# Optimization experiments

Hardware: AMD Instinct MI355X
Metric: run time of the kernel (lower is better)

The kernel has to match this reference:

```python
import jax, jax.numpy as jnp
import numpy as np

N_NODES = 500_000
N_EDGES = 16_000_000


def setup_inputs() -> dict:
    key = jax.random.key(0)
    ks = jax.random.split(key, 16)
    x = jax.random.normal(ks[0], (N_NODES, 4), dtype=jnp.float32)
    edge_index = jax.random.randint(ks[1], (2, N_EDGES), 0, N_NODES, dtype=jnp.int64)

    def lin(k, out_dim, in_dim):
        # kaiming-uniform-ish init like torch Linear
        bound = 1.0 / np.sqrt(in_dim)
        return jax.random.uniform(k, (out_dim, in_dim), jnp.float32, -bound, bound)

    def bias(k, out_dim, in_dim):
        bound = 1.0 / np.sqrt(in_dim)
        return jax.random.uniform(k, (out_dim,), jnp.float32, -bound, bound)

    return {
        "x": x,
        "edge_index": edge_index,
        # SAGEConv1: 4 -> 10  (lin_l acts on aggregated neighbors, has bias; lin_r on self, no bias)
        "w1l": lin(ks[2], 10, 4), "b1": bias(ks[3], 10, 4), "w1r": lin(ks[4], 10, 4),
        # SAGEConv2: 10 -> 20
        "w2l": lin(ks[5], 20, 10), "b2": bias(ks[6], 20, 10), "w2r": lin(ks[7], 20, 10),
        # SAGEConv3: 20 -> 20
        "w3l": lin(ks[8], 20, 20), "b3": bias(ks[9], 20, 20), "w3r": lin(ks[10], 20, 20),
        # classifier: 20 -> 8
        "wc": lin(ks[11], 8, 20), "bc": bias(ks[12], 8, 20),
    }


def _sage_conv(h, src, dst, deg_inv, wl, bl, wr):
    # mean-aggregate neighbor features: messages flow src -> dst
    msg = h[src]                                   # [E, F] gather
    agg = jax.ops.segment_sum(msg, dst, num_segments=N_NODES)  # [N, F]
    agg = agg * deg_inv                            # mean over in-neighbors
    return agg @ wl.T + bl + h @ wr.T              # lin_l(aggr) + lin_r(self)


def reference(x, edge_index, w1l, b1, w1r, w2l, b2, w2r, w3l, b3, w3r, wc, bc):
    src, dst = edge_index[0], edge_index[1]
    deg = jax.ops.segment_sum(jnp.ones((src.shape[0],), x.dtype), dst,
                              num_segments=N_NODES)
    deg_inv = (1.0 / jnp.maximum(deg, 1.0))[:, None]  # [N, 1]

    h = jax.nn.relu(_sage_conv(x, src, dst, deg_inv, w1l, b1, w1r))
    h = jax.nn.relu(_sage_conv(h, src, dst, deg_inv, w2l, b2, w2r))
    h = jax.nn.relu(_sage_conv(h, src, dst, deg_inv, w3l, b3, w3r))
    return h @ wc.T + bc
```

## Files before the change

### kernel.cpp

```cpp
#include <hip/hip_runtime.h>
#include <hip/hip_fp16.h>

#define N_NODES 500000
#define N_EDGES 16000000
#define NB 1954
#define NPB_LOG 9
#define NPB 512
#define NBUCK 977
#define NBUCK_PAD 1024
#define CH 16384
#define NSB 977

#define SLICE_SHIFT 15
#define NSLICE 16
#define NKEY (NPB * NSLICE)

#define GRID_BLK 1024
#define HALF_T (GRID_BLK * 256)

#define BAR_SUBC 16
#define BAR_SUBQ (GRID_BLK / BAR_SUBC)
#define BAR_REC_INTS 1024
#define BAR_MASTER 512
#define BAR_FLAG 544
#define ENTRY_BUDGET 1500
#define PHASE_BUDGET 400

__device__ __forceinline__ float2 up2(int p) {
    __half2 h = *reinterpret_cast<__half2*>(&p);
    return __half22float2(h);
}
__device__ __forceinline__ int pk2(float a, float b) {
    __half2 h = __floats2half2_rn(a, b);
    return *reinterpret_cast<int*>(&h);
}

__device__ __forceinline__ void barrier_arrive(int* rec, int bid) {
    int r = __hip_atomic_fetch_add(&rec[(bid & (BAR_SUBC - 1)) * 32], 1,
                                   __ATOMIC_RELAXED, __HIP_MEMORY_SCOPE_AGENT);
    if (r == BAR_SUBQ - 1) {
        int mr = __hip_atomic_fetch_add(&rec[BAR_MASTER], 1,
                                        __ATOMIC_RELAXED, __HIP_MEMORY_SCOPE_AGENT);
        if (mr == BAR_SUBC - 1)
            __hip_atomic_store(&rec[BAR_FLAG], 1,
                               __ATOMIC_RELAXED, __HIP_MEMORY_SCOPE_AGENT);
    }
}
__device__ __forceinline__ bool barrier_wait(int* rec, int budget) {
    int spins = 0;
    while (__hip_atomic_load(&rec[BAR_FLAG],
                             __ATOMIC_RELAXED, __HIP_MEMORY_SCOPE_AGENT) == 0) {
        if (++spins > budget) return false;
        __builtin_amdgcn_s_sleep(8);
    }
    return true;
}


__global__ void bucket_hist(const int* __restrict__ dst, int* __restrict__ ghist) {
    __shared__ int lhist[NBUCK_PAD];
    for (int t = threadIdx.x; t < NBUCK_PAD; t += 256) lhist[t] = 0;
    __syncthreads();
    int stride = gridDim.x * 256;
    for (int i = blockIdx.x * 256 + threadIdx.x; i < N_EDGES; i += stride) {
        atomicAdd(&lhist[dst[i] >> NPB_LOG], 1);
    }
    __syncthreads();
    for (int t = threadIdx.x; t < NBUCK_PAD; t += 256) {
        int c = lhist[t];
        if (c) atomicAdd(&ghist[t], c);
    }
}

__global__ void bucket_scan(int* __restrict__ gcur, int* __restrict__ bbase) {
    __shared__ int s[256];
    int t = threadIdx.x;
    int v[4], sum = 0, loc[4];
#pragma unroll
    for (int j = 0; j < 4; ++j) {
        v[j] = gcur[t * 4 + j];
        loc[j] = sum;
        sum += v[j];
    }
    s[t] = sum;
    __syncthreads();
    for (int o = 1; o < 256; o <<= 1) {
        int x = (t >= o) ? s[t - o] : 0;
        __syncthreads();
        s[t] += x;
        __syncthreads();
    }
    int excl = s[t] - sum;
#pragma unroll
    for (int j = 0; j < 4; ++j) {
        int e = excl + loc[j];
        bbase[t * 4 + j] = e;
        gcur[t * 4 + j] = e;
    }
    if (t == 255) bbase[NBUCK_PAD] = s[255];
}

__global__ __launch_bounds__(256) void bucket_scatter(
        const int* __restrict__ src, const int* __restrict__ dst,
        int* __restrict__ gcur, int* __restrict__ P) {
    __shared__ int lP[CH];
    __shared__ int lhist[NBUCK_PAD];
    __shared__ int lexcl[NBUCK_PAD];
    __shared__ int gbase[NBUCK_PAD];
    __shared__ int sscan[256];
    int t = threadIdx.x;
    for (int j = t; j < NBUCK_PAD; j += 256) lhist[j] = 0;
    __syncthreads();

    int e0 = blockIdx.x * CH;
    int e1 = min(e0 + CH, N_EDGES);
    for (int i = e0 + t; i < e1; i += 256) {
        atomicAdd(&lhist[dst[i] >> NPB_LOG], 1);
    }
    __syncthreads();

    int base4 = t * 4;
    int c[4], sum = 0;
#pragma unroll
    for (int j = 0; j < 4; ++j) { c[j] = lhist[base4 + j]; sum += c[j]; }
#pragma unroll
    for (int j = 0; j < 4; ++j) {
        gbase[base4 + j] = c[j] ? atomicAdd(&gcur[base4 + j], c[j]) : 0;
    }
    sscan[t] = sum;
    __syncthreads();
    for (int o = 1; o < 256; o <<= 1) {
        int x = (t >= o) ? sscan[t - o] : 0;
        __syncthreads();
        sscan[t] += x;
        __syncthreads();
    }
    int run = sscan[t] - sum;
#pragma unroll
    for (int j = 0; j < 4; ++j) {
        lexcl[base4 + j] = run;
        lhist[base4 + j] = run;
        run += c[j];
    }
    __syncthreads();

    for (int i = e0 + t; i < e1; i += 256) {
        int d = dst[i];
        int s = src[i];
        int b = d >> NPB_LOG;
        int pos = atomicAdd(&lhist[b], 1);
        lP[pos] = ((d & (NPB - 1)) << 19) | s;
    }
    __syncthreads();

    int wave = t >> 6, lane = t & 63;
    for (int b = wave; b < NBUCK_PAD; b += 4) {
        int lb = lexcl[b];
        int cnt = lhist[b] - lb;
        int gb = gbase[b];
        for (int j = lane; j < cnt; j += 64) {
            P[gb + j] = lP[lb + j];
        }
    }
}

__global__ void fine_sort(const int* __restrict__ P, const int* __restrict__ bbase,
                          int* __restrict__ off, int* __restrict__ S) {
    __shared__ int hist[NKEY];
    __shared__ int sscan[256];
    int t = threadIdx.x;
    int b = blockIdx.x;
    int bb = bbase[b];
    int be = bbase[b + 1];
    int node0 = b << NPB_LOG;

    for (int j = t; j < NKEY; j += 256) hist[j] = 0;
    __syncthreads();
    for (int j = bb + t; j < be; j += 256) {
        int p = P[j];
        int n = p >> 19;
        int s = p & 0x7FFFF;
        atomicAdd(&hist[(n << 4) | (s >> SLICE_SHIFT)], 1);
    }
    __syncthreads();

    int base = t * 32;
    int sum = 0;
#pragma unroll
    for (int j = 0; j < 32; ++j) sum += hist[base + j];
    sscan[t] = sum;
    __syncthreads();
    for (int o = 1; o < 256; o <<= 1) {
        int x = (t >= o) ? sscan[t - o] : 0;
        __syncthreads();
        sscan[t] += x;
        __syncthreads();
    }
    int run = sscan[t] - sum;
#pragma unroll
    for (int j = 0; j < 32; ++j) {
        int c = hist[base + j];
        hist[base + j] = run;
        run += c;
    }
    __syncthreads();

#pragma unroll
    for (int j = 0; j < 2; ++j) {
        int idx = t + j * 256;
        int ng = node0 + idx;
        if (ng < N_NODES) off[ng] = bb + hist[idx << 4];
    }
    if (b == NBUCK - 1 && t == 0) off[N_NODES] = N_EDGES;
    __syncthreads();

    for (int j = bb + t; j < be; j += 256) {
        int p = P[j];
        int n = p >> 19;
        int s = p & 0x7FFFF;
        int pos = atomicAdd(&hist[(n << 4) | (s >> SLICE_SHIFT)], 1);
        S[bb + pos] = s;
    }
}

__global__ __launch_bounds__(256) void count_slices(const int* __restrict__ off,
        const int* __restrict__ S, int4* __restrict__ cnt8) {
    int i = blockIdx.x * 256 + threadIdx.x;
    if (i >= N_NODES) return;
    int b = off[i], e = off[i + 1];
    int w0 = 0, w1 = 0, w2 = 0, w3 = 0;
    for (int k = b; k < e; ++k) {
        int sl = S[k] >> SLICE_SHIFT;
        int inc = 1 << ((sl & 3) * 8);
        if (sl < 8) { if (sl < 4) w0 += inc; else w1 += inc; }
        else        { if (sl < 12) w2 += inc; else w3 += inc; }
    }
    cnt8[i] = make_int4(w0, w1, w2, w3);
}


__global__ void convert_x(const float* __restrict__ x, int2* __restrict__ xh) {
    int i = blockIdx.x * 256 + threadIdx.x;
    if (i >= N_NODES) return;
    float4 v = ((const float4*)x)[i];
    int2 r;
    r.x = pk2(v.x, v.y);
    r.y = pk2(v.z, v.w);
    xh[i] = r;
}


__global__ __launch_bounds__(256, 4) void fused_l1(
        const int* __restrict__ off, const int* __restrict__ ssrc,
        const int2* __restrict__ xh, const float* __restrict__ x,
        const float* __restrict__ wl, const float* __restrict__ bl,
        const float* __restrict__ wr, int* __restrict__ h1) {
    __shared__ float s_wl[40];
    __shared__ float s_wr[40];
    __shared__ float s_b[10];
    if (threadIdx.x < 40) {
        s_wl[threadIdx.x] = wl[threadIdx.x];
        s_wr[threadIdx.x] = wr[threadIdx.x];
    }
    if (threadIdx.x >= 64 && threadIdx.x < 74) s_b[threadIdx.x - 64] = bl[threadIdx.x - 64];
    __syncthreads();

    int i = blockIdx.x * 256 + threadIdx.x;
    if (i >= N_NODES) return;

    int b = off[i], e = off[i + 1];
    constexpr int UN = 8;

    float acc[4] = {0.f, 0.f, 0.f, 0.f};

    int k = b;
    for (; k + UN - 1 < e; k += UN) {
        int sidx[UN];
#pragma unroll
        for (int u = 0; u < UN; ++u) sidx[u] = ssrc[k + u];
        int2 v[UN];
#pragma unroll
        for (int u = 0; u < UN; ++u) v[u] = xh[sidx[u]];
#pragma unroll
        for (int u = 0; u < UN; ++u) {
            float2 f0 = up2(v[u].x), f1 = up2(v[u].y);
            acc[0] += f0.x; acc[1] += f0.y; acc[2] += f1.x; acc[3] += f1.y;
        }
    }
    for (; k < e; ++k) {
        int2 v = xh[ssrc[k]];
        float2 f0 = up2(v.x), f1 = up2(v.y);
        acc[0] += f0.x; acc[1] += f0.y; acc[2] += f1.x; acc[3] += f1.y;
    }

    float inv = 1.f / fmaxf((float)(e - b), 1.f);
#pragma unroll
    for (int q = 0; q < 4; ++q) acc[q] *= inv;

    float4 xs = ((const float4*)x)[i];
    float xv[4] = {xs.x, xs.y, xs.z, xs.w};

    float r[10];
#pragma unroll
    for (int j = 0; j < 10; ++j) {
        float t = s_b[j];
#pragma unroll
        for (int kk = 0; kk < 4; ++kk) {
            t += s_wl[j * 4 + kk] * acc[kk] + s_wr[j * 4 + kk] * xv[kk];
        }
        r[j] = fmaxf(t, 0.f);
    }
    int4 o0;
    o0.x = pk2(r[0], r[1]); o0.y = pk2(r[2], r[3]);
    o0.z = pk2(r[4], r[5]); o0.w = pk2(r[6], r[7]);
    *(int4*)(h1 + (long)i * 8) = o0;
    h1[(long)i * 8 + 4] = pk2(r[8], r[9]);
}


__device__ __forceinline__ void l2_scan_m(int& k, int m,
        const int* __restrict__ ssrc, const int* __restrict__ h1, float* acc) {
    for (; m >= 4; m -= 4, k += 4) {
        int sidx[4];
#pragma unroll
        for (int u = 0; u < 4; ++u) sidx[u] = ssrc[k + u];
        int4 v4[4];
        int v1[4];
#pragma unroll
        for (int u = 0; u < 4; ++u) {
            const int* row = h1 + (long)sidx[u] * 8;
            v4[u] = *(const int4*)row;
            v1[u] = row[4];
        }
#pragma unroll
        for (int u = 0; u < 4; ++u) {
            float2 f0 = up2(v4[u].x), f1 = up2(v4[u].y), f2 = up2(v4[u].z),
                   f3 = up2(v4[u].w), f4 = up2(v1[u]);
            acc[0] += f0.x; acc[1] += f0.y; acc[2] += f1.x; acc[3] += f1.y;
            acc[4] += f2.x; acc[5] += f2.y; acc[6] += f3.x; acc[7] += f3.y;
            acc[8] += f4.x; acc[9] += f4.y;
        }
    }
    for (; m > 0; --m, ++k) {
        const int* row = h1 + (long)ssrc[k] * 8;
        int4 v4 = *(const int4*)row;
        int v1 = row[4];
        float2 f0 = up2(v4.x), f1 = up2(v4.y), f2 = up2(v4.z), f3 = up2(v4.w), f4 = up2(v1);
        acc[0] += f0.x; acc[1] += f0.y; acc[2] += f1.x; acc[3] += f1.y;
        acc[4] += f2.x; acc[5] += f2.y; acc[6] += f3.x; acc[7] += f3.y;
        acc[8] += f4.x; acc[9] += f4.y;
    }
}

__device__ __forceinline__ void l3_scan_m(int& k, int m,
        const int* __restrict__ ssrc, const int* __restrict__ h2, float* acc) {
    for (; m >= 4; m -= 4, k += 4) {
        int sidx[4];
#pragma unroll
        for (int u = 0; u < 4; ++u) sidx[u] = ssrc[k + u];
        int4 va[4], vb[4];
        int2 vc[4];
#pragma unroll
        for (int u = 0; u < 4; ++u) {
            const int* row = h2 + (long)sidx[u] * 16;
            va[u] = *(const int4*)row;
            vb[u] = *(const int4*)(row + 4);
            vc[u] = *(const int2*)(row + 8);
        }
#pragma unroll
        for (int u = 0; u < 4; ++u) {
            float2 f;
            f = up2(va[u].x); acc[0] += f.x; acc[1] += f.y;
            f = up2(va[u].y); acc[2] += f.x; acc[3] += f.y;
            f = up2(va[u].z); acc[4] += f.x; acc[5] += f.y;
            f = up2(va[u].w); acc[6] += f.x; acc[7] += f.y;
            f = up2(vb[u].x); acc[8] += f.x; acc[9] += f.y;
            f = up2(vb[u].y); acc[10] += f.x; acc[11] += f.y;
            f = up2(vb[u].z); acc[12] += f.x; acc[13] += f.y;
            f = up2(vb[u].w); acc[14] += f.x; acc[15] += f.y;
            f = up2(vc[u].x); acc[16] += f.x; acc[17] += f.y;
            f = up2(vc[u].y); acc[18] += f.x; acc[19] += f.y;
        }
    }
    for (; m > 0; --m, ++k) {
        const int* row = h2 + (long)ssrc[k] * 16;
        int4 va = *(const int4*)row;
        int4 vb = *(const int4*)(row + 4);
        int2 vc = *(const int2*)(row + 8);
        float2 f;
        f = up2(va.x); acc[0] += f.x; acc[1] += f.y;
        f = up2(va.y); acc[2] += f.x; acc[3] += f.y;
        f = up2(va.z); acc[4] += f.x; acc[5] += f.y;
        f = up2(va.w); acc[6] += f.x; acc[7] += f.y;
        f = up2(vb.x); acc[8] += f.x; acc[9] += f.y;
        f = up2(vb.y); acc[10] += f.x; acc[11] += f.y;
        f = up2(vb.z); acc[12] += f.x; acc[13] += f.y;
        f = up2(vb.w); acc[14] += f.x; acc[15] += f.y;
        f = up2(vc.x); acc[16] += f.x; acc[17] += f.y;
        f = up2(vc.y); acc[18] += f.x; acc[19] += f.y;
    }
}

__device__ __forceinline__ void l2_tail(int n, float deg, float* acc,
        const int* __restrict__ h1, const float* s_wl, const float* s_wr,
        const float* s_b, int* __restrict__ h2) {
    if (n >= N_NODES) return;
    float inv = 1.f / fmaxf(deg, 1.f);
#pragma unroll
    for (int q = 0; q < 10; ++q) acc[q] *= inv;
    float xv[10];
    {
        const int* row = h1 + (long)n * 8;
        int4 v4 = *(const int4*)row;
        int v1 = row[4];
        float2 f0 = up2(v4.x), f1 = up2(v4.y), f2 = up2(v4.z), f3 = up2(v4.w), f4 = up2(v1);
        xv[0] = f0.x; xv[1] = f0.y; xv[2] = f1.x; xv[3] = f1.y;
        xv[4] = f2.x; xv[5] = f2.y; xv[6] = f3.x; xv[7] = f3.y;
        xv[8] = f4.x; xv[9] = f4.y;
    }
    float r[20];
#pragma unroll
    for (int j = 0; j < 20; ++j) {
        float t = s_b[j];
#pragma unroll
        for (int kk = 0; kk < 10; ++kk)
            t += s_wl[j * 10 + kk] * acc[kk] + s_wr[j * 10 + kk] * xv[kk];
        r[j] = fmaxf(t, 0.f);
    }
    int* o = h2 + (long)n * 16;
    int4 o0, o1;
    o0.x = pk2(r[0], r[1]);   o0.y = pk2(r[2], r[3]);
    o0.z = pk2(r[4], r[5]);   o0.w = pk2(r[6], r[7]);
    o1.x = pk2(r[8], r[9]);   o1.y = pk2(r[10], r[11]);
    o1.z = pk2(r[12], r[13]); o1.w = pk2(r[14], r[15]);
    *(int4*)o = o0;
    *(int4*)(o + 4) = o1;
    int2 o2;
    o2.x = pk2(r[16], r[17]); o2.y = pk2(r[18], r[19]);
    *(int2*)(o + 8) = o2;
}

__global__ __launch_bounds__(256, 4) void fused_l2p(
        const int* __restrict__ off, const int* __restrict__ ssrc,
        const int* __restrict__ h1,
        const float* __restrict__ wl, const float* __restrict__ bl,
        const float* __restrict__ wr, int* __restrict__ h2,
        const int4* __restrict__ cnt8, int* __restrict__ bar) {
    __shared__ float s_wl[200];
    __shared__ float s_wr[200];
    __shared__ float s_b[20];
    if (threadIdx.x < 200) {
        s_wl[threadIdx.x] = wl[threadIdx.x];
        s_wr[threadIdx.x] = wr[threadIdx.x];
    }
    if (threadIdx.x >= 224 && threadIdx.x < 244) s_b[threadIdx.x - 224] = bl[threadIdx.x - 224];
    __syncthreads();

    const int tg = blockIdx.x * 256 + threadIdx.x;
    const int n0 = tg, n1 = tg + HALF_T;
    int k0 = off[n0];
    float deg0 = (float)(off[n0 + 1] - k0);
    int4 c0 = cnt8[n0];
    int k1 = 0;
    float deg1 = 0.f;
    int4 c1 = make_int4(0, 0, 0, 0);
    if (n1 < N_NODES) {
        k1 = off[n1];
        deg1 = (float)(off[n1 + 1] - k1);
        c1 = cnt8[n1];
    }
    float acc0[10], acc1[10];
#pragma unroll
    for (int q = 0; q < 10; ++q) { acc0[q] = 0.f; acc1[q] = 0.f; }

    bool coop = true;
    if (threadIdx.x == 0) {
        barrier_arrive(bar, blockIdx.x);
        coop = barrier_wait(bar, ENTRY_BUDGET);
    }
    __syncthreads();

    constexpr int PH = 8;
    for (int s = 0; s < PH; ++s) {
        int cw0 = (s < 4) ? ((s < 2) ? c0.x : c0.y) : ((s < 6) ? c0.z : c0.w);
        int cw1 = (s < 4) ? ((s < 2) ? c1.x : c1.y) : ((s < 6) ? c1.z : c1.w);
        int sh = (s & 1) * 16;
        int m0 = ((cw0 >> sh) & 255) + ((cw0 >> (sh + 8)) & 255);
        int m1 = ((cw1 >> sh) & 255) + ((cw1 >> (sh + 8)) & 255);
        l2_scan_m(k0, m0, ssrc, h1, acc0);
        l2_scan_m(k1, m1, ssrc, h1, acc1);
        if (s < PH - 1) {
            if (threadIdx.x == 0) {
                int* rec = bar + (1 + s) * BAR_REC_INTS;
                barrier_arrive(rec, blockIdx.x);
                if (coop) coop = barrier_wait(rec, PHASE_BUDGET);
            }
            __syncthreads();
        }
    }
    l2_tail(n0, deg0, acc0, h1, s_wl, s_wr, s_b, h2);
    l2_tail(n1, deg1, acc1, h1, s_wl, s_wr, s_b, h2);
}

__device__ __forceinline__ void l3_tail(int n, float deg, float* acc,
        const int* __restrict__ h2, const float* s_wl, const float* s_wr,
        const float* s_b, const float* s_wc, const float* s_bc,
        float* __restrict__ out) {
    if (n >= N_NODES) return;
    float inv = 1.f / fmaxf(deg, 1.f);
#pragma unroll
    for (int q = 0; q < 20; ++q) acc[q] *= inv;
    float xv[20];
    {
        const int* row = h2 + (long)n * 16;
        int4 va = *(const int4*)row;
        int4 vb = *(const int4*)(row + 4);
        int2 vc = *(const int2*)(row + 8);
        float2 f;
        f = up2(va.x); xv[0] = f.x; xv[1] = f.y;
        f = up2(va.y); xv[2] = f.x; xv[3] = f.y;
        f = up2(va.z); xv[4] = f.x; xv[5] = f.y;
        f = up2(va.w); xv[6] = f.x; xv[7] = f.y;
        f = up2(vb.x); xv[8] = f.x; xv[9] = f.y;
        f = up2(vb.y); xv[10] = f.x; xv[11] = f.y;
        f = up2(vb.z); xv[12] = f.x; xv[13] = f.y;
        f = up2(vb.w); xv[14] = f.x; xv[15] = f.y;
        f = up2(vc.x); xv[16] = f.x; xv[17] = f.y;
        f = up2(vc.y); xv[18] = f.x; xv[19] = f.y;
    }
    float h3[20];
#pragma unroll
    for (int j = 0; j < 20; ++j) {
        float r = s_b[j];
#pragma unroll
        for (int kk = 0; kk < 20; ++kk)
            r += s_wl[j * 20 + kk] * acc[kk] + s_wr[j * 20 + kk] * xv[kk];
        h3[j] = fmaxf(r, 0.f);
    }
#pragma unroll
    for (int j = 0; j < 8; ++j) {
        float r = s_bc[j];
#pragma unroll
        for (int kk = 0; kk < 20; ++kk) r += s_wc[j * 20 + kk] * h3[kk];
        out[(long)n * 8 + j] = r;
    }
}

__global__ __launch_bounds__(256, 4) void fused_l3p(
        const int* __restrict__ off, const int* __restrict__ ssrc,
        const int* __restrict__ h2,
        const float* __restrict__ w3l, const float* __restrict__ b3,
        const float* __restrict__ w3r,
        const float* __restrict__ wc, const float* __restrict__ bc,
        float* __restrict__ out, const int4* __restrict__ cnt8,
        int* __restrict__ bar) {
    __shared__ float s_wl[400];
    __shared__ float s_wr[400];
    __shared__ float s_b[20];
    __shared__ float s_wc[160];
    __shared__ float s_bc[8];
    for (int t = threadIdx.x; t < 400; t += 256) {
        s_wl[t] = w3l[t];
        s_wr[t] = w3r[t];
    }
    if (threadIdx.x < 160) s_wc[threadIdx.x] = wc[threadIdx.x];
    if (threadIdx.x >= 192 && threadIdx.x < 212) s_b[threadIdx.x - 192] = b3[threadIdx.x - 192];
    if (threadIdx.x >= 224 && threadIdx.x < 232) s_bc[threadIdx.x - 224] = bc[threadIdx.x - 224];
    __syncthreads();

    const int tg = blockIdx.x * 256 + threadIdx.x;
    const int n0 = tg, n1 = tg + HALF_T;
    int k0 = off[n0];
    float deg0 = (float)(off[n0 + 1] - k0);
    int4 c0 = cnt8[n0];
    int k1 = 0;
    float deg1 = 0.f;
    int4 c1 = make_int4(0, 0, 0, 0);
    if (n1 < N_NODES) {
        k1 = off[n1];
        deg1 = (float)(off[n1 + 1] - k1);
        c1 = cnt8[n1];
    }
    float acc0[20], acc1[20];
#pragma unroll
    for (int q = 0; q < 20; ++q) { acc0[q] = 0.f; acc1[q] = 0.f; }

    bool coop = true;
    if (threadIdx.x == 0) {
        barrier_arrive(bar, blockIdx.x);
        coop = barrier_wait(bar, ENTRY_BUDGET);
    }
    __syncthreads();

    constexpr int PH = 16;
    for (int s = 0; s < PH; ++s) {
        int cw0 = (s < 8) ? ((s < 4) ? c0.x : c0.y) : ((s < 12) ? c0.z : c0.w);
        int cw1 = (s < 8) ? ((s < 4) ? c1.x : c1.y) : ((s < 12) ? c1.z : c1.w);
        int sh = (s & 3) * 8;
        int m0 = (cw0 >> sh) & 255;
        int m1 = (cw1 >> sh) & 255;
        l3_scan_m(k0, m0, ssrc, h2, acc0);
        l3_scan_m(k1, m1, ssrc, h2, acc1);
        if (s < PH - 1) {
            if (threadIdx.x == 0) {
                int* rec = bar + (1 + s) * BAR_REC_INTS;
                barrier_arrive(rec, blockIdx.x);
                if (coop) coop = barrier_wait(rec, PHASE_BUDGET);
            }
            __syncthreads();
        }
    }
    l3_tail(n0, deg0, acc0, h2, s_wl, s_wr, s_b, s_wc, s_bc, out);
    l3_tail(n1, deg1, acc1, h2, s_wl, s_wr, s_b, s_wc, s_bc, out);
}


__global__ void deg_kernel(const int* __restrict__ dst, int* __restrict__ deg) {
    int i = blockIdx.x * blockDim.x + threadIdx.x;
    if (i < N_EDGES) atomicAdd(&deg[dst[i]], 1);
}

template <int F>
__global__ void edge_agg(const int* __restrict__ src, const int* __restrict__ dst,
                         const float* __restrict__ h, float* __restrict__ agg) {
    int i = blockIdx.x * blockDim.x + threadIdx.x;
    if (i >= N_EDGES) return;
    int s = src[i];
    int d = dst[i];
    const float* hs = h + (long)s * F;
    float* ad = agg + (long)d * F;
#pragma unroll
    for (int f = 0; f < F; ++f) atomicAdd(&ad[f], hs[f]);
}

template <int FIN, int FOUT>
__global__ void node_apply(const float* __restrict__ agg, const float* __restrict__ hin,
                           const int* __restrict__ deg, const float* __restrict__ wl,
                           const float* __restrict__ bl, const float* __restrict__ wr,
                           float* __restrict__ hout) {
    __shared__ float s_wl[FOUT * FIN];
    __shared__ float s_wr[FOUT * FIN];
    __shared__ float s_b[FOUT];
    for (int t = threadIdx.x; t < FOUT * FIN; t += blockDim.x) {
        s_wl[t] = wl[t];
        s_wr[t] = wr[t];
    }
    for (int t = threadIdx.x; t < FOUT; t += blockDim.x) s_b[t] = bl[t];
    __syncthreads();
    int i = blockIdx.x * blockDim.x + threadIdx.x;
    if (i >= N_NODES) return;
    float inv = 1.0f / fmaxf((float)deg[i], 1.0f);
    float a[FIN], xv[FIN];
#pragma unroll
    for (int kk = 0; kk < FIN; ++kk) {
        a[kk] = agg[(long)i * FIN + kk] * inv;
        xv[kk] = hin[(long)i * FIN + kk];
    }
#pragma unroll
    for (int j = 0; j < FOUT; ++j) {
        float r = s_b[j];
#pragma unroll
        for (int kk = 0; kk < FIN; ++kk) r += s_wl[j * FIN + kk] * a[kk] + s_wr[j * FIN + kk] * xv[kk];
        hout[(long)i * FOUT + j] = fmaxf(r, 0.f);
    }
}

__global__ void node_final_old(const float* __restrict__ agg, const float* __restrict__ hin,
                               const int* __restrict__ deg, const float* __restrict__ w3l,
                               const float* __restrict__ b3, const float* __restrict__ w3r,
                               const float* __restrict__ wc, const float* __restrict__ bc,
                               float* __restrict__ out) {
    __shared__ float s_wl[400];
    __shared__ float s_wr[400];
    __shared__ float s_b[20];
    __shared__ float s_wc[160];
    __shared__ float s_bc[8];
    for (int t = threadIdx.x; t < 400; t += blockDim.x) {
        s_wl[t] = w3l[t];
        s_wr[t] = w3r[t];
    }
    for (int t = threadIdx.x; t < 160; t += blockDim.x) s_wc[t] = wc[t];
    for (int t = threadIdx.x; t < 20; t += blockDim.x) s_b[t] = b3[t];
    for (int t = threadIdx.x; t < 8; t += blockDim.x) s_bc[t] = bc[t];
    __syncthreads();
    int i = blockIdx.x * blockDim.x + threadIdx.x;
    if (i >= N_NODES) return;
    float inv = 1.0f / fmaxf((float)deg[i], 1.0f);
    float a[20], xv[20];
#pragma unroll
    for (int kk = 0; kk < 20; ++kk) {
        a[kk] = agg[(long)i * 20 + kk] * inv;
        xv[kk] = hin[(long)i * 20 + kk];
    }
    float h3[20];
#pragma unroll
    for (int j = 0; j < 20; ++j) {
        float r = s_b[j];
#pragma unroll
        for (int kk = 0; kk < 20; ++kk) r += s_wl[j * 20 + kk] * a[kk] + s_wr[j * 20 + kk] * xv[kk];
        h3[j] = fmaxf(r, 0.f);
    }
#pragma unroll
    for (int j = 0; j < 8; ++j) {
        float r = s_bc[j];
#pragma unroll
        for (int kk = 0; kk < 20; ++kk) r += s_wc[j * 20 + kk] * h3[kk];
        out[(long)i * 8 + j] = r;
    }
}


extern "C" void kernel_launch(void* const* d_in, const int* in_sizes, int n_in,
                              void* d_out, int out_size, void* d_ws, size_t ws_size,
                              hipStream_t stream) {
    const float* x = (const float*)d_in[0];
    const int* ei = (const int*)d_in[1];
    const float* w1l = (const float*)d_in[2];
    const float* b1 = (const float*)d_in[3];
    const float* w1r = (const float*)d_in[4];
    const float* w2l = (const float*)d_in[5];
    const float* b2 = (const float*)d_in[6];
    const float* w2r = (const float*)d_in[7];
    const float* w3l = (const float*)d_in[8];
    const float* b3 = (const float*)d_in[9];
    const float* w3r = (const float*)d_in[10];
    const float* wc = (const float*)d_in[11];
    const float* bc = (const float*)d_in[12];
    float* out = (float*)d_out;

    const int* src = ei;
    const int* dst = ei + N_EDGES;

    const int BT = 256;
    dim3 blk(BT);
    dim3 egrid((N_EDGES + BT - 1) / BT);
    dim3 ngrid(NB);

    const size_t NEED_A = 130008448;

    if (ws_size >= NEED_A) {
        char* ws = (char*)d_ws;
        int* off = (int*)ws;
        int* bbase = (int*)(ws + 2000128);
        int* gcur = (int*)(ws + 2004352);
        int* P = (int*)(ws + 2008448);
        int2* xh = (int2*)(ws + 2008448);
        int* h1 = (int*)(ws + 6008448);
        int* h2 = (int*)(ws + 22008448);
        int* bar2 = (int*)(ws + 54008448);
        int* bar3 = bar2 + 8 * BAR_REC_INTS;
        int4* cnt8 = (int4*)(ws + 54206464);
        int* S = (int*)(ws + 66008448);

        hipMemsetAsync(gcur, 0, NBUCK_PAD * sizeof(int), stream);
        bucket_hist<<<1024, blk, 0, stream>>>(dst, gcur);
        bucket_scan<<<1, blk, 0, stream>>>(gcur, bbase);
        bucket_scatter<<<NSB, blk, 0, stream>>>(src, dst, gcur, P);
        fine_sort<<<NBUCK, blk, 0, stream>>>(P, bbase, off, S);

        hipMemsetAsync(bar2, 0, 24 * BAR_REC_INTS * sizeof(int), stream);

        count_slices<<<ngrid, blk, 0, stream>>>(off, S, cnt8);
        convert_x<<<ngrid, blk, 0, stream>>>(x, xh);
        fused_l1<<<ngrid, blk, 0, stream>>>(off, S, xh, x, w1l, b1, w1r, h1);
        fused_l2p<<<GRID_BLK, blk, 0, stream>>>(off, S, h1, w2l, b2, w2r, h2, cnt8, bar2);
        fused_l3p<<<GRID_BLK, blk, 0, stream>>>(off, S, h2, w3l, b3, w3r, wc, bc, out, cnt8, bar3);
    } else {
        char* ws = (char*)d_ws;
        int* deg = (int*)ws;
        float* agg = (float*)(ws + 2000000);
        float* h1 = (float*)(ws + 42000000);
        float* h2 = (float*)(ws + 62000000);

        hipMemsetAsync(deg, 0, (size_t)N_NODES * sizeof(int), stream);
        deg_kernel<<<egrid, blk, 0, stream>>>(dst, deg);

        hipMemsetAsync(agg, 0, (size_t)N_NODES * 4 * sizeof(float), stream);
        edge_agg<4><<<egrid, blk, 0, stream>>>(src, dst, x, agg);
        node_apply<4, 10><<<ngrid, blk, 0, stream>>>(agg, x, deg, w1l, b1, w1r, h1);

        hipMemsetAsync(agg, 0, (size_t)N_NODES * 10 * sizeof(float), stream);
        edge_agg<10><<<egrid, blk, 0, stream>>>(src, dst, h1, agg);
        node_apply<10, 20><<<ngrid, blk, 0, stream>>>(agg, h1, deg, w2l, b2, w2r, h2);

        hipMemsetAsync(agg, 0, (size_t)N_NODES * 20 * sizeof(float), stream);
        edge_agg<20><<<egrid, blk, 0, stream>>>(src, dst, h2, agg);
        node_final_old<<<ngrid, blk, 0, stream>>>(agg, h2, deg, w3l, b3, w3r, wc, bc, out);
    }
}
```

Baseline: 1.494 ms.

## Split packed hidden features into SoA planes and halve grid-barrier phase count

Stores the fp16-packed hidden features h1 and h2 as separate arrays per chunk (int4 plus int, and int4, int4, int2) instead of one padded interleaved row per node. Each gathered chunk array is denser, which may improve cache-line use for the random neighbour gathers. It also merges slice groups so layer 2 runs 4 barrier phases instead of 8 and layer 3 runs 8 instead of 16, cutting grid-wide barrier overhead. In exchange each phase covers a wider source-node range, so the gathers lose some cache locality, and each gather now issues several separate memory transactions per row.

```diff
diff --git a/kernel.cpp b/kernel.cpp
--- a/kernel.cpp
+++ b/kernel.cpp
@@ -254,7 +254,8 @@
         const int* __restrict__ off, const int* __restrict__ ssrc,
         const int2* __restrict__ xh, const float* __restrict__ x,
         const float* __restrict__ wl, const float* __restrict__ bl,
-        const float* __restrict__ wr, int* __restrict__ h1) {
+        const float* __restrict__ wr,
+        int4* __restrict__ h1a, int* __restrict__ h1b) {
     __shared__ float s_wl[40];
     __shared__ float s_wr[40];
     __shared__ float s_b[10];
@@ -313,13 +314,14 @@
     int4 o0;
     o0.x = pk2(r[0], r[1]); o0.y = pk2(r[2], r[3]);
     o0.z = pk2(r[4], r[5]); o0.w = pk2(r[6], r[7]);
-    *(int4*)(h1 + (long)i * 8) = o0;
-    h1[(long)i * 8 + 4] = pk2(r[8], r[9]);
+    h1a[i] = o0;
+    h1b[i] = pk2(r[8], r[9]);
 }
 
 
 __device__ __forceinline__ void l2_scan_m(int& k, int m,
-        const int* __restrict__ ssrc, const int* __restrict__ h1, float* acc) {
+        const int* __restrict__ ssrc, const int4* __restrict__ h1a,
+        const int* __restrict__ h1b, float* acc) {
     for (; m >= 4; m -= 4, k += 4) {
         int sidx[4];
 #pragma unroll
@@ -328,9 +330,8 @@
         int v1[4];
 #pragma unroll
         for (int u = 0; u < 4; ++u) {
-            const int* row = h1 + (long)sidx[u] * 8;
-            v4[u] = *(const int4*)row;
-            v1[u] = row[4];
+            v4[u] = h1a[sidx[u]];
+            v1[u] = h1b[sidx[u]];
         }
 #pragma unroll
         for (int u = 0; u < 4; ++u) {
@@ -342,9 +343,9 @@
         }
     }
     for (; m > 0; --m, ++k) {
-        const int* row = h1 + (long)ssrc[k] * 8;
-        int4 v4 = *(const int4*)row;
-        int v1 = row[4];
+        int s = ssrc[k];
+        int4 v4 = h1a[s];
+        int v1 = h1b[s];
         float2 f0 = up2(v4.x), f1 = up2(v4.y), f2 = up2(v4.z), f3 = up2(v4.w), f4 = up2(v1);
         acc[0] += f0.x; acc[1] += f0.y; acc[2] += f1.x; acc[3] += f1.y;
         acc[4] += f2.x; acc[5] += f2.y; acc[6] += f3.x; acc[7] += f3.y;
@@ -353,7 +354,8 @@
 }
 
 __device__ __forceinline__ void l3_scan_m(int& k, int m,
-        const int* __restrict__ ssrc, const int* __restrict__ h2, float* acc) {
+        const int* __restrict__ ssrc, const int4* __restrict__ h2a,
+        const int4* __restrict__ h2b, const int2* __restrict__ h2c, float* acc) {
     for (; m >= 4; m -= 4, k += 4) {
         int sidx[4];
 #pragma unroll
@@ -362,10 +364,9 @@
         int2 vc[4];
 #pragma unroll
         for (int u = 0; u < 4; ++u) {
-            const int* row = h2 + (long)sidx[u] * 16;
-            va[u] = *(const int4*)row;
-            vb[u] = *(const int4*)(row + 4);
-            vc[u] = *(const int2*)(row + 8);
+            va[u] = h2a[sidx[u]];
+            vb[u] = h2b[sidx[u]];
+            vc[u] = h2c[sidx[u]];
         }
 #pragma unroll
         for (int u = 0; u < 4; ++u) {
@@ -383,10 +384,10 @@
         }
     }
     for (; m > 0; --m, ++k) {
-        const int* row = h2 + (long)ssrc[k] * 16;
-        int4 va = *(const int4*)row;
-        int4 vb = *(const int4*)(row + 4);
-        int2 vc = *(const int2*)(row + 8);
+        int s = ssrc[k];
+        int4 va = h2a[s];
+        int4 vb = h2b[s];
+        int2 vc = h2c[s];
         float2 f;
         f = up2(va.x); acc[0] += f.x; acc[1] += f.y;
         f = up2(va.y); acc[2] += f.x; acc[3] += f.y;
@@ -402,17 +403,17 @@
 }
 
 __device__ __forceinline__ void l2_tail(int n, float deg, float* acc,
-        const int* __restrict__ h1, const float* s_wl, const float* s_wr,
-        const float* s_b, int* __restrict__ h2) {
+        const int4* __restrict__ h1a, const int* __restrict__ h1b,
+        const float* s_wl, const float* s_wr, const float* s_b,
+        int4* __restrict__ h2a, int4* __restrict__ h2b, int2* __restrict__ h2c) {
     if (n >= N_NODES) return;
     float inv = 1.f / fmaxf(deg, 1.f);
 #pragma unroll
     for (int q = 0; q < 10; ++q) acc[q] *= inv;
     float xv[10];
     {
-        const int* row = h1 + (long)n * 8;
-        int4 v4 = *(const int4*)row;
-        int v1 = row[4];
+        int4 v4 = h1a[n];
+        int v1 = h1b[n];
         float2 f0 = up2(v4.x), f1 = up2(v4.y), f2 = up2(v4.z), f3 = up2(v4.w), f4 = up2(v1);
         xv[0] = f0.x; xv[1] = f0.y; xv[2] = f1.x; xv[3] = f1.y;
         xv[4] = f2.x; xv[5] = f2.y; xv[6] = f3.x; xv[7] = f3.y;
@@ -427,24 +428,24 @@
             t += s_wl[j * 10 + kk] * acc[kk] + s_wr[j * 10 + kk] * xv[kk];
         r[j] = fmaxf(t, 0.f);
     }
-    int* o = h2 + (long)n * 16;
     int4 o0, o1;
     o0.x = pk2(r[0], r[1]);   o0.y = pk2(r[2], r[3]);
     o0.z = pk2(r[4], r[5]);   o0.w = pk2(r[6], r[7]);
     o1.x = pk2(r[8], r[9]);   o1.y = pk2(r[10], r[11]);
     o1.z = pk2(r[12], r[13]); o1.w = pk2(r[14], r[15]);
-    *(int4*)o = o0;
-    *(int4*)(o + 4) = o1;
+    h2a[n] = o0;
+    h2b[n] = o1;
     int2 o2;
     o2.x = pk2(r[16], r[17]); o2.y = pk2(r[18], r[19]);
-    *(int2*)(o + 8) = o2;
+    h2c[n] = o2;
 }
 
 __global__ __launch_bounds__(256, 4) void fused_l2p(
         const int* __restrict__ off, const int* __restrict__ ssrc,
-        const int* __restrict__ h1,
+        const int4* __restrict__ h1a, const int* __restrict__ h1b,
         const float* __restrict__ wl, const float* __restrict__ bl,
-        const float* __restrict__ wr, int* __restrict__ h2,
+        const float* __restrict__ wr,
+        int4* __restrict__ h2a, int4* __restrict__ h2b, int2* __restrict__ h2c,
         const int4* __restrict__ cnt8, int* __restrict__ bar) {
     __shared__ float s_wl[200];
     __shared__ float s_wr[200];
@@ -480,15 +481,14 @@
     }
     __syncthreads();
 
-    constexpr int PH = 8;
+    constexpr int PH = 4;
     for (int s = 0; s < PH; ++s) {
-        int cw0 = (s < 4) ? ((s < 2) ? c0.x : c0.y) : ((s < 6) ? c0.z : c0.w);
-        int cw1 = (s < 4) ? ((s < 2) ? c1.x : c1.y) : ((s < 6) ? c1.z : c1.w);
-        int sh = (s & 1) * 16;
-        int m0 = ((cw0 >> sh) & 255) + ((cw0 >> (sh + 8)) & 255);
-        int m1 = ((cw1 >> sh) & 255) + ((cw1 >> (sh + 8)) & 255);
-        l2_scan_m(k0, m0, ssrc, h1, acc0);
-        l2_scan_m(k1, m1, ssrc, h1, acc1);
+        int cw0 = (s < 2) ? ((s < 1) ? c0.x : c0.y) : ((s < 3) ? c0.z : c0.w);
+        int cw1 = (s < 2) ? ((s < 1) ? c1.x : c1.y) : ((s < 3) ? c1.z : c1.w);
+        int m0 = (cw0 & 255) + ((cw0 >> 8) & 255) + ((cw0 >> 16) & 255) + ((cw0 >> 24) & 255);
+        int m1 = (cw1 & 255) + ((cw1 >> 8) & 255) + ((cw1 >> 16) & 255) + ((cw1 >> 24) & 255);
+        l2_scan_m(k0, m0, ssrc, h1a, h1b, acc0);
+        l2_scan_m(k1, m1, ssrc, h1a, h1b, acc1);
         if (s < PH - 1) {
             if (threadIdx.x == 0) {
                 int* rec = bar + (1 + s) * BAR_REC_INTS;
@@ -498,12 +498,14 @@
             __syncthreads();
         }
     }
-    l2_tail(n0, deg0, acc0, h1, s_wl, s_wr, s_b, h2);
-    l2_tail(n1, deg1, acc1, h1, s_wl, s_wr, s_b, h2);
+    l2_tail(n0, deg0, acc0, h1a, h1b, s_wl, s_wr, s_b, h2a, h2b, h2c);
+    l2_tail(n1, deg1, acc1, h1a, h1b, s_wl, s_wr, s_b, h2a, h2b, h2c);
 }
 
 __device__ __forceinline__ void l3_tail(int n, float deg, float* acc,
-        const int* __restrict__ h2, const float* s_wl, const float* s_wr,
+        const int4* __restrict__ h2a, const int4* __restrict__ h2b,
+        const int2* __restrict__ h2c,
+        const float* s_wl, const float* s_wr,
         const float* s_b, const float* s_wc, const float* s_bc,
         float* __restrict__ out) {
     if (n >= N_NODES) return;
@@ -512,10 +514,9 @@
     for (int q = 0; q < 20; ++q) acc[q] *= inv;
     float xv[20];
     {
-        const int* row = h2 + (long)n * 16;
-        int4 va = *(const int4*)row;
-        int4 vb = *(const int4*)(row + 4);
-        int2 vc = *(const int2*)(row + 8);
+        int4 va = h2a[n];
+        int4 vb = h2b[n];
+        int2 vc = h2c[n];
         float2 f;
         f = up2(va.x); xv[0] = f.x; xv[1] = f.y;
         f = up2(va.y); xv[2] = f.x; xv[3] = f.y;
@@ -548,7 +549,8 @@
 
 __global__ __launch_bounds__(256, 4) void fused_l3p(
         const int* __restrict__ off, const int* __restrict__ ssrc,
-        const int* __restrict__ h2,
+        const int4* __restrict__ h2a, const int4* __restrict__ h2b,
+        const int2* __restrict__ h2c,
         const float* __restrict__ w3l, const float* __restrict__ b3,
         const float* __restrict__ w3r,
         const float* __restrict__ wc, const float* __restrict__ bc,
@@ -592,15 +594,15 @@
     }
     __syncthreads();
 
-    constexpr int PH = 16;
+    constexpr int PH = 8;
     for (int s = 0; s < PH; ++s) {
-        int cw0 = (s < 8) ? ((s < 4) ? c0.x : c0.y) : ((s < 12) ? c0.z : c0.w);
-        int cw1 = (s < 8) ? ((s < 4) ? c1.x : c1.y) : ((s < 12) ? c1.z : c1.w);
-        int sh = (s & 3) * 8;
-        int m0 = (cw0 >> sh) & 255;
-        int m1 = (cw1 >> sh) & 255;
-        l3_scan_m(k0, m0, ssrc, h2, acc0);
-        l3_scan_m(k1, m1, ssrc, h2, acc1);
+        int cw0 = (s < 4) ? ((s < 2) ? c0.x : c0.y) : ((s < 6) ? c0.z : c0.w);
+        int cw1 = (s < 4) ? ((s < 2) ? c1.x : c1.y) : ((s < 6) ? c1.z : c1.w);
+        int sh = (s & 1) * 16;
+        int m0 = ((cw0 >> sh) & 255) + ((cw0 >> (sh + 8)) & 255);
+        int m1 = ((cw1 >> sh) & 255) + ((cw1 >> (sh + 8)) & 255);
+        l3_scan_m(k0, m0, ssrc, h2a, h2b, h2c, acc0);
+        l3_scan_m(k1, m1, ssrc, h2a, h2b, h2c, acc1);
         if (s < PH - 1) {
             if (threadIdx.x == 0) {
                 int* rec = bar + (1 + s) * BAR_REC_INTS;
@@ -610,8 +612,8 @@
             __syncthreads();
         }
     }
-    l3_tail(n0, deg0, acc0, h2, s_wl, s_wr, s_b, s_wc, s_bc, out);
-    l3_tail(n1, deg1, acc1, h2, s_wl, s_wr, s_b, s_wc, s_bc, out);
+    l3_tail(n0, deg0, acc0, h2a, h2b, h2c, s_wl, s_wr, s_b, s_wc, s_bc, out);
+    l3_tail(n1, deg1, acc1, h2a, h2b, h2c, s_wl, s_wr, s_b, s_wc, s_bc, out);
 }
 
 
@@ -745,8 +747,11 @@
         int* gcur = (int*)(ws + 2004352);
         int* P = (int*)(ws + 2008448);
         int2* xh = (int2*)(ws + 2008448);
-        int* h1 = (int*)(ws + 6008448);
-        int* h2 = (int*)(ws + 22008448);
+        int4* h1a = (int4*)(ws + 6008448);
+        int* h1b = (int*)(ws + 14008448);
+        int4* h2a = (int4*)(ws + 16008448);
+        int4* h2b = (int4*)(ws + 24008448);
+        int2* h2c = (int2*)(ws + 32008448);
         int* bar2 = (int*)(ws + 54008448);
         int* bar3 = bar2 + 8 * BAR_REC_INTS;
         int4* cnt8 = (int4*)(ws + 54206464);
@@ -762,9 +767,11 @@
 
         count_slices<<<ngrid, blk, 0, stream>>>(off, S, cnt8);
         convert_x<<<ngrid, blk, 0, stream>>>(x, xh);
-        fused_l1<<<ngrid, blk, 0, stream>>>(off, S, xh, x, w1l, b1, w1r, h1);
-        fused_l2p<<<GRID_BLK, blk, 0, stream>>>(off, S, h1, w2l, b2, w2r, h2, cnt8, bar2);
-        fused_l3p<<<GRID_BLK, blk, 0, stream>>>(off, S, h2, w3l, b3, w3r, wc, bc, out, cnt8, bar3);
+        fused_l1<<<ngrid, blk, 0, stream>>>(off, S, xh, x, w1l, b1, w1r, h1a, h1b);
+        fused_l2p<<<GRID_BLK, blk, 0, stream>>>(off, S, h1a, h1b, w2l, b2, w2r,
+                                                h2a, h2b, h2c, cnt8, bar2);
+        fused_l3p<<<GRID_BLK, blk, 0, stream>>>(off, S, h2a, h2b, h2c,
+                                                w3l, b3, w3r, wc, bc, out, cnt8, bar3);
     } else {
         char* ws = (char*)d_ws;
         int* deg = (int*)ws;
```

New measurement: 1.525 ms. 1.02x slower.
